# Kernel optimization log

Measured on AMD Instinct MI355X. Metric: run time of the kernel, lower is better.

Reference implementation:

```python
import jax, jax.numpy as jnp
import numpy as np

BETA = 5.0
NEG = jnp.float32(-1e30)  # finite stand-in for -inf; avoids NaN on the fully-masked row 0


def setup_inputs() -> dict:
    key = jax.random.key(0)
    ks = jax.random.split(key, 6)
    B, L, d, dv, dh = 4, 4096, 512, 512, 512
    K = jax.random.normal(ks[0], (B, L, d), dtype=jnp.float32)
    V = jax.random.normal(ks[1], (B, L, dv), dtype=jnp.float32)
    # nn.Linear weights: shape (out, in), applied as x @ W.T
    Wq = jax.random.normal(ks[2], (dh, d), dtype=jnp.float32) / np.sqrt(d).astype(np.float32)
    Wk = jax.random.normal(ks[3], (dh, d), dtype=jnp.float32) / np.sqrt(d).astype(np.float32)
    Wv = jax.random.normal(ks[4], (dv, dv), dtype=jnp.float32) / np.sqrt(dv).astype(np.float32)
    Wo = jax.random.normal(ks[5], (dv, dv), dtype=jnp.float32) / np.sqrt(dv).astype(np.float32)
    return {"K": K, "V": V, "Wq": Wq, "Wk": Wk, "Wv": Wv, "Wo": Wo}


def reference(K, V, Wq, Wk, Wv, Wo):
    B, L, _ = K.shape
    dh = Wq.shape[0]
    Qh = jnp.einsum('bld,hd->blh', K, Wq)
    Kh = jnp.einsum('bld,hd->blh', K, Wk)
    Vp = jnp.einsum('bld,ed->ble', V, Wv)
    scale = jnp.float32(BETA) / jnp.sqrt(jnp.float32(dh))
    scores = jnp.einsum('bih,bjh->bij', Qh, Kh) * scale  # [B,L,L]
    # strict causal mask: attend only to j <= i-1 (triu with diagonal=0 masked)
    mask = jnp.triu(jnp.ones((L, L), dtype=bool), k=0)
    scores = jnp.where(mask[None], NEG, scores)
    attn = jax.nn.softmax(scores, axis=-1)
    # row 0 has no past: torch code zeroes it after softmax
    attn = attn.at[:, 0, :].set(0.0)
    out = jnp.einsum('bij,bjd->bid', attn, Vp)
    Vhat = jnp.einsum('bld,ed->ble', out, Wo)
    return Vhat
```

## Files before the change

kernel.cpp:

```cpp
#include <hip/hip_runtime.h>


typedef unsigned short u16;
typedef _Float16 f16;
typedef short short8 __attribute__((ext_vector_type(8)));
typedef _Float16 half8 __attribute__((ext_vector_type(8)));
typedef _Float16 half4 __attribute__((ext_vector_type(4)));
typedef float floatx4 __attribute__((ext_vector_type(4)));

#define L_SEQ 4096
#define NBATCH 4
#define DMODEL 512
#define SCALE 0.22097086912079612f
#define MMAX 30.0f

__device__ __forceinline__ u16 f2bf(float f) {
  unsigned int u = __float_as_uint(f);
  u += 0x7fffu + ((u >> 16) & 1u);
  return (u16)(u >> 16);
}
__device__ __forceinline__ float bf2f(u16 h) {
  return __uint_as_float(((unsigned int)h) << 16);
}

__device__ __forceinline__ void gl2lds16(const void* g, void* l) {
  __builtin_amdgcn_global_load_lds(
      (const __attribute__((address_space(1))) unsigned int*)g,
      (__attribute__((address_space(3))) unsigned int*)l, 16, 0, 0);
}

__global__ __launch_bounds__(256) void cvt_f16_x4b(
    const float4* __restrict__ x0, half4* __restrict__ o0,
    const float4* __restrict__ x1, half4* __restrict__ o1, int n4a,
    const float4* __restrict__ x2, half4* __restrict__ o2,
    const float4* __restrict__ x3, half4* __restrict__ o3, int n4b) {
  int i = blockIdx.x * 256 + threadIdx.x;
  int y = blockIdx.y;
  const float4* __restrict__ x;
  half4* __restrict__ o;
  int n4;
  if (y == 0)      { x = x0; o = o0; n4 = n4a; }
  else if (y == 1) { x = x1; o = o1; n4 = n4a; }
  else if (y == 2) { x = x2; o = o2; n4 = n4b; }
  else             { x = x3; o = o3; n4 = n4b; }
  if (i >= n4) return;
  float4 f = x[i];
  half4 h = {(f16)f.x, (f16)f.y, (f16)f.z, (f16)f.w};
  o[i] = h;
}

__global__ __launch_bounds__(256) void cvt_t16(
    const float* __restrict__ x0, f16* __restrict__ o0,
    const float* __restrict__ x1, f16* __restrict__ o1) {
  const float* __restrict__ x = blockIdx.z ? x1 : x0;
  f16* __restrict__ o = blockIdx.z ? o1 : o0;
  __shared__ f16 t[64][72];
  const int r0 = blockIdx.y * 64, c0 = blockIdx.x * 64;
  const int tr = threadIdx.x >> 4, tc4 = (threadIdx.x & 15) * 4;
#pragma unroll
  for (int it = 0; it < 4; it++) {
    int r = tr + it * 16;
    float4 v = *(const float4*)&x[(long)(r0 + r) * 512 + c0 + tc4];
    t[tc4 + 0][r] = (f16)v.x;
    t[tc4 + 1][r] = (f16)v.y;
    t[tc4 + 2][r] = (f16)v.z;
    t[tc4 + 3][r] = (f16)v.w;
  }
  __syncthreads();
  const int wr = threadIdx.x >> 3, wc8 = (threadIdx.x & 7) * 8;
#pragma unroll
  for (int it = 0; it < 2; it++) {
    int rr = wr + it * 32;
    half8 h;
#pragma unroll
    for (int e = 0; e < 8; e++) h[e] = t[rr][wc8 + e];
    *(half8*)&o[(long)(c0 + rr) * 512 + r0 + wc8] = h;
  }
}

template <int OUT_MODE>
__global__ __launch_bounds__(256, 2) void gemm128(
    const f16* __restrict__ A, const f16* __restrict__ B,
    void* __restrict__ Cout, int ldc, long sAz, long sBz, long sCz) {
  __shared__ f16 sA[2][128 * 64];
  __shared__ f16 sB[2][128 * 64];

  const int tid = threadIdx.x;
  const int wave = tid >> 6, lane = tid & 63, quad = lane >> 4, l16 = lane & 15;
  const int wm = (wave >> 1) * 64, wn = (wave & 1) * 64;
  const int bn = blockIdx.x * 128, bm = blockIdx.y * 128, bz = blockIdx.z;

  const f16* Ab = A + (long)bz * sAz + (long)bm * 512;
  const f16* Bb = B + (long)bz * sBz + (long)bn * 512;

  floatx4 zero = {0.f, 0.f, 0.f, 0.f};
  floatx4 acc[4][4];
#pragma unroll
  for (int mi = 0; mi < 4; mi++)
#pragma unroll
    for (int ni = 0; ni < 4; ni++) acc[mi][ni] = zero;

  const int lrow = lane >> 3;
  auto stage = [&](int bs, int ks) {
#pragma unroll
    for (int i = 0; i < 4; i++) {
      int r0 = wave * 32 + i * 8;
      int r = r0 + lrow;
      int c = ((lane & 7) - r) & 7;
      gl2lds16(Ab + (long)r * 512 + ks * 64 + c * 8, &sA[bs][r0 * 64]);
      gl2lds16(Bb + (long)r * 512 + ks * 64 + c * 8, &sB[bs][r0 * 64]);
    }
  };

  stage(0, 0);
  for (int ks = 0; ks < 8; ks++) {
    const int cur = ks & 1;
    __syncthreads();
    if (ks + 1 < 8) stage(cur ^ 1, ks + 1);

#pragma unroll
    for (int kk = 0; kk < 2; kk++) {
      half8 af[4], bf[4];
#pragma unroll
      for (int mi = 0; mi < 4; mi++) {
        int row = wm + mi * 16 + l16;
        int slot = (kk * 4 + quad + row) & 7;
        af[mi] = *(const half8*)&sA[cur][row * 64 + slot * 8];
      }
#pragma unroll
      for (int ni = 0; ni < 4; ni++) {
        int row = wn + ni * 16 + l16;
        int slot = (kk * 4 + quad + row) & 7;
        bf[ni] = *(const half8*)&sB[cur][row * 64 + slot * 8];
      }
#pragma unroll
      for (int mi = 0; mi < 4; mi++)
#pragma unroll
        for (int ni = 0; ni < 4; ni++)
          acc[mi][ni] = __builtin_amdgcn_mfma_f32_16x16x32_f16(
              af[mi], bf[ni], acc[mi][ni], 0, 0, 0);
    }
  }

#pragma unroll
  for (int mi = 0; mi < 4; mi++) {
#pragma unroll
    for (int ni = 0; ni < 4; ni++) {
#pragma unroll
      for (int rr = 0; rr < 4; rr++) {
        int row = bm + wm + mi * 16 + quad * 4 + rr;
        int col = bn + wn + ni * 16 + l16;
        long idx = (long)bz * sCz + (long)row * ldc + col;
        float v = acc[mi][ni][rr];
        if (OUT_MODE == 1) {
          ((f16*)Cout)[idx] = (f16)v;
        } else if (OUT_MODE == 3) {
          ((u16*)Cout)[idx] = f2bf(v);
        } else {
          ((float*)Cout)[idx] = v;
        }
      }
    }
  }
}

__device__ __forceinline__ int nseg_of(int qt) {
  return (qt < 12) ? ((qt + 2) >> 1) : ((qt + 4) >> 2);
}
__device__ __forceinline__ int seg_off(int qt) {
  int o = 0;
  for (int q = 2; q < qt; q++) o += 4 * nseg_of(q);
  return o;
}

#define SV_LD 40

__global__ __launch_bounds__(512, 2) void attn_kernel(
    const f16* __restrict__ Qh_g, const f16* __restrict__ Kh_g,
    const u16* __restrict__ VpT, f16* __restrict__ Ob,
    u16* __restrict__ Opart, float* __restrict__ ml) {
  __shared__ f16 sK[2][32 * 512];
  __shared__ u16 sV[2][512 * 32];
  __shared__ u16 sP[8 * 16 * SV_LD];
  __shared__ float sL[128];

  const int tid = threadIdx.x;
  const int wave = tid >> 6, lane = tid & 63, quad = lane >> 4, l16 = lane & 15;

  int id = blockIdx.x;
  int qt = 31;
  for (;;) {
    int c = 4 * nseg_of(qt);
    if (id < c) break;
    id -= c;
    qt--;
  }
  const int S = nseg_of(qt);
  const int b = id / S;
  const int s = id - b * S;
  const int ktn = 4 * qt + 4;
  const int base = ktn / S, rem = ktn - base * S;
  const int len = base + (s < rem);
  const int start = s * base + (s < rem ? s : rem);

  const int q0 = qt * 128 + wave * 16;
  const long qbase = (long)b * L_SEQ + q0;

  half8 qf[16];
#pragma unroll
  for (int c = 0; c < 16; c++) {
    long a = (qbase + l16) * 512 + c * 32 + quad * 8;
    qf[c] = *(const half8*)&Qh_g[a];
  }

  floatx4 zero = {0.f, 0.f, 0.f, 0.f};
  float l_run[4] = {0.f, 0.f, 0.f, 0.f};
  floatx4 oacc[32];
#pragma unroll
  for (int nb = 0; nb < 32; nb++) oacc[nb] = zero;

  const f16* __restrict__ Kh_b = Kh_g + (long)b * L_SEQ * 512;
  const u16* __restrict__ V_b  = VpT + (long)b * (512L * L_SEQ);

  auto stage = [&](int bs, int jt) {
    const int j0 = jt * 32;
#pragma unroll
    for (int i = 0; i < 4; i++) {
      int r = wave * 4 + i;
      int k = (lane - (r & 7)) & 63;
      gl2lds16(Kh_b + (long)(j0 + r) * 512 + k * 8, &sK[bs][r * 512]);
    }
#pragma unroll
    for (int i = 0; i < 4; i++) {
      int g = wave * 4 + i;
      int d = g * 16 + (lane >> 2);
      int c = ((lane & 3) - (d + (d >> 2))) & 3;
      gl2lds16(V_b + (long)d * L_SEQ + j0 + c * 8, &sV[bs][g * 512]);
    }
  };

  stage(0, start);

  for (int v = 0; v < len; v++) {
    const int j0 = (start + v) * 32;
    const int cur = v & 1;

    __syncthreads();
    if (v + 1 < len) stage(cur ^ 1, start + v + 1);

    const f16* kc = &sK[cur][0];
    const u16* vc = &sV[cur][0];

    floatx4 sacc0 = zero, sacc1 = zero;
    const int rot = l16 & 7;
#pragma unroll
    for (int c = 0; c < 16; c++) {
      int slot = (c * 4 + quad + rot) & 63;
      half8 b0 = *(const half8*)&kc[l16 * 512 + slot * 8];
      half8 b1 = *(const half8*)&kc[(16 + l16) * 512 + slot * 8];
      sacc0 = __builtin_amdgcn_mfma_f32_16x16x32_f16(qf[c], b0, sacc0, 0, 0, 0);
      sacc1 = __builtin_amdgcn_mfma_f32_16x16x32_f16(qf[c], b1, sacc1, 0, 0, 0);
    }

#pragma unroll
    for (int rr = 0; rr < 4; rr++) {
      int irow = q0 + quad * 4 + rr;
      float s0 = fmaf(sacc0[rr], SCALE, -MMAX);
      float s1 = fmaf(sacc1[rr], SCALE, -MMAX);
      if (j0 + l16 >= irow) s0 = -1e30f;
      if (j0 + 16 + l16 >= irow) s1 = -1e30f;
      float p0 = __expf(s0);
      float p1 = __expf(s1);
      l_run[rr] += p0 + p1;
      int pb = wave * (16 * SV_LD) + (quad * 4 + rr) * SV_LD;
      sP[pb + l16] = f2bf(p0);
      sP[pb + 16 + l16] = f2bf(p1);
    }

    __builtin_amdgcn_sched_barrier(0);
    __builtin_amdgcn_s_waitcnt(0xC07F);
    __builtin_amdgcn_s_barrier();
    __builtin_amdgcn_sched_barrier(0);

    short8 vf[4];
#pragma unroll
    for (int nbl = 0; nbl < 4; nbl++) {
      int dvr = wave * 64 + nbl * 16 + l16;
      vf[nbl] = *(const short8*)&vc[dvr * 32 + ((quad + l16 + (l16 >> 2)) & 3) * 8];
    }
#pragma unroll
    for (int qg = 0; qg < 8; qg++) {
      short8 ap = *(const short8*)&sP[qg * (16 * SV_LD) + l16 * SV_LD + quad * 8];
#pragma unroll
      for (int nbl = 0; nbl < 4; nbl++)
        oacc[qg * 4 + nbl] =
            __builtin_amdgcn_mfma_f32_16x16x32_bf16(ap, vf[nbl], oacc[qg * 4 + nbl], 0, 0, 0);
    }
  }

#pragma unroll
  for (int rr = 0; rr < 4; rr++) {
    float l = l_run[rr];
    l += __shfl_xor(l, 1);
    l += __shfl_xor(l, 2);
    l += __shfl_xor(l, 4);
    l += __shfl_xor(l, 8);
    l_run[rr] = l;
  }
  if (l16 == 0) {
#pragma unroll
    for (int rr = 0; rr < 4; rr++) sL[wave * 16 + quad * 4 + rr] = l_run[rr];
  }
  __syncthreads();

  if (S == 1) {
#pragma unroll
    for (int qg = 0; qg < 8; qg++) {
#pragma unroll
      for (int rr = 0; rr < 4; rr++) {
        int row = qg * 16 + quad * 4 + rr;
        int irow = qt * 128 + row;
        float lv = sL[row];
        float inv = (irow == 0 || lv <= 0.f) ? 0.f : 1.0f / lv;
        long obase = ((long)b * L_SEQ + irow) * 512 + wave * 64;
#pragma unroll
        for (int nbl = 0; nbl < 4; nbl++)
          Ob[obase + nbl * 16 + l16] = (f16)(oacc[qg * 4 + nbl][rr] * inv);
      }
    }
  } else {
    const int slot = seg_off(qt) + b * S + s;
    const long obase0 = (long)slot * (128 * 512);
#pragma unroll
    for (int qg = 0; qg < 8; qg++) {
#pragma unroll
      for (int rr = 0; rr < 4; rr++) {
        int row = qg * 16 + quad * 4 + rr;
        long ob = obase0 + (long)row * 512 + wave * 64;
#pragma unroll
        for (int nbl = 0; nbl < 4; nbl++)
          Opart[ob + nbl * 16 + l16] = f2bf(oacc[qg * 4 + nbl][rr]);
      }
    }
    if (l16 == 0) {
#pragma unroll
      for (int rr = 0; rr < 4; rr++)
        ml[slot * 128 + wave * 16 + quad * 4 + rr] = l_run[rr];
    }
  }
}

__global__ __launch_bounds__(256) void attn_combine(
    const u16* __restrict__ Opart, const float* __restrict__ ml,
    f16* __restrict__ Ob) {
  const int qt = 2 + (blockIdx.x >> 2), b = blockIdx.x & 3;
  const int S = nseg_of(qt);
  const int bslot = seg_off(qt) + b * S;
  __shared__ float sInv[128];
  const int tid = threadIdx.x;
  if (tid < 128) {
    int row = tid, irow = qt * 128 + row;
    float ltot = 0.f;
    for (int s = 0; s < S; s++) ltot += ml[(bslot + s) * 128 + row];
    sInv[row] = (irow == 0 || ltot <= 0.f) ? 0.f : 1.0f / ltot;
  }
  __syncthreads();
  const int c0 = blockIdx.y * 16;
  for (int idx = tid; idx < 128 * 16; idx += 256) {
    int row = idx >> 4, cc = c0 + (idx & 15);
    float acc[8] = {0, 0, 0, 0, 0, 0, 0, 0};
    for (int s = 0; s < S; s++) {
      int4 pk = *(const int4*)&Opart[(long)(bslot + s) * 65536 + row * 512 + cc * 8];
      const u16* ph = (const u16*)&pk;
#pragma unroll
      for (int e = 0; e < 8; e++) acc[e] += bf2f(ph[e]);
    }
    float inv = sInv[row];
    f16 o[8];
#pragma unroll
    for (int e = 0; e < 8; e++) o[e] = (f16)(acc[e] * inv);
    *(int4*)&Ob[((long)b * L_SEQ + qt * 128 + row) * 512 + cc * 8] = *(int4*)o;
  }
}

extern "C" void kernel_launch(void* const* d_in, const int* in_sizes, int n_in,
                              void* d_out, int out_size, void* d_ws, size_t ws_size,
                              hipStream_t stream) {
  const float* K  = (const float*)d_in[0];
  const float* V  = (const float*)d_in[1];
  const float* Wq = (const float*)d_in[2];
  const float* Wk = (const float*)d_in[3];
  const float* Wv = (const float*)d_in[4];
  const float* Wo = (const float*)d_in[5];
  float* out = (float*)d_out;

  const int NKV = NBATCH * L_SEQ * DMODEL;
  const int NW = DMODEL * DMODEL;
  const int NSLOT = 640;

  char* w = (char*)d_ws;
  size_t off = 0;
  auto carve = [&](size_t bytes) {
    void* p = w + off;
    off += (bytes + 255) & ~(size_t)255;
    return p;
  };
  f16* Qh   = (f16*)carve((size_t)NKV * 2);
  f16* K16  = (f16*)carve((size_t)NKV * 2);
  u16* VpTw = (u16*)carve((size_t)NKV * 2);
  f16* Obw  = (f16*)carve((size_t)NKV * 2);
  f16* Wo16 = (f16*)carve((size_t)NW * 2);
  f16* MTw  = (f16*)carve((size_t)NW * 2);
  float* mlw = (float*)carve((size_t)NSLOT * 128 * 4);
  u16* Opart = (u16*)carve((size_t)NSLOT * 65536 * 2);
  f16* V16   = (f16*)Opart;
  f16* WqT16 = V16 + NKV;
  f16* WkT16 = WqT16 + NW;
  f16* Wv16  = WkT16 + NW;

  cvt_f16_x4b<<<dim3(NKV / 1024, 4, 1), 256, 0, stream>>>(
      (const float4*)K, (half4*)K16, (const float4*)V, (half4*)V16, NKV / 4,
      (const float4*)Wv, (half4*)Wv16, (const float4*)Wo, (half4*)Wo16, NW / 4);
  cvt_t16<<<dim3(8, 8, 2), 256, 0, stream>>>(Wq, WqT16, Wk, WkT16);

  gemm128<1><<<dim3(4, 4, 1), 256, 0, stream>>>(
      WkT16, WqT16, (void*)MTw, 512, 0, 0, 0);

  gemm128<1><<<dim3(4, 128, 1), 256, 0, stream>>>(
      K16, MTw, (void*)Qh, 512, 0, 0, 0);

  gemm128<3><<<dim3(32, 4, NBATCH), 256, 0, stream>>>(
      Wv16, V16, (void*)VpTw, L_SEQ, 0, (long)L_SEQ * 512, (long)512 * L_SEQ);

  attn_kernel<<<dim3(648, 1, 1), 512, 0, stream>>>(
      Qh, K16, VpTw, Obw, Opart, mlw);
  attn_combine<<<dim3(120, 4, 1), 256, 0, stream>>>(Opart, mlw, Obw);

  gemm128<2><<<dim3(4, 128, 1), 256, 0, stream>>>(
      Obw, Wo16, (void*)out, 512, 0, 0, 0);

  (void)in_sizes; (void)n_in; (void)out_size; (void)ws_size;
}
```

Measured before the change: 350.2 us.

## Fuse split-KV combine into attention via atomic counters and merge projection GEMMs

Removes the separate attn_combine launch: the last-arriving segment block for each (query tile, batch) detects completion with an atomic counter after a threadfence and performs the reduction itself. It also merges the Qh and Vp^T projection GEMMs into one grid, and moves the small weight conversions plus counter reset into one kernel. Fewer launches and better tail filling are the goal. The cost is an atomic, extra fences, and serialized reduction work on the last block per group.

```diff
diff --git a/kernel.cpp b/kernel.cpp
--- a/kernel.cpp
+++ b/kernel.cpp
@@ -29,34 +29,41 @@
       (__attribute__((address_space(3))) unsigned int*)l, 16, 0, 0);
 }
 
-__global__ __launch_bounds__(256) void cvt_f16_x4b(
+__global__ __launch_bounds__(256) void cvt_big(
     const float4* __restrict__ x0, half4* __restrict__ o0,
-    const float4* __restrict__ x1, half4* __restrict__ o1, int n4a,
-    const float4* __restrict__ x2, half4* __restrict__ o2,
-    const float4* __restrict__ x3, half4* __restrict__ o3, int n4b) {
+    const float4* __restrict__ x1, half4* __restrict__ o1, int n4) {
   int i = blockIdx.x * 256 + threadIdx.x;
-  int y = blockIdx.y;
-  const float4* __restrict__ x;
-  half4* __restrict__ o;
-  int n4;
-  if (y == 0)      { x = x0; o = o0; n4 = n4a; }
-  else if (y == 1) { x = x1; o = o1; n4 = n4a; }
-  else if (y == 2) { x = x2; o = o2; n4 = n4b; }
-  else             { x = x3; o = o3; n4 = n4b; }
   if (i >= n4) return;
+  const float4* __restrict__ x = blockIdx.y ? x1 : x0;
+  half4* __restrict__ o = blockIdx.y ? o1 : o0;
   float4 f = x[i];
   half4 h = {(f16)f.x, (f16)f.y, (f16)f.z, (f16)f.w};
   o[i] = h;
 }
 
-__global__ __launch_bounds__(256) void cvt_t16(
-    const float* __restrict__ x0, f16* __restrict__ o0,
-    const float* __restrict__ x1, f16* __restrict__ o1) {
-  const float* __restrict__ x = blockIdx.z ? x1 : x0;
-  f16* __restrict__ o = blockIdx.z ? o1 : o0;
+__global__ __launch_bounds__(256) void cvt_small(
+    const float* __restrict__ Wv, f16* __restrict__ Wv16,
+    const float* __restrict__ Wo, f16* __restrict__ Wo16,
+    const float* __restrict__ Wq, f16* __restrict__ WqT16,
+    const float* __restrict__ Wk, f16* __restrict__ WkT16,
+    int* __restrict__ cnt) {
   __shared__ f16 t[64][72];
-  const int r0 = blockIdx.y * 64, c0 = blockIdx.x * 64;
-  const int tr = threadIdx.x >> 4, tc4 = (threadIdx.x & 15) * 4;
+  const int y = blockIdx.y, bx = blockIdx.x, tid = threadIdx.x;
+  if (y == 0 && bx == 0 && tid < 128) cnt[tid] = 0;
+  if (y < 2) {
+    const float4* __restrict__ x = (const float4*)(y ? Wo : Wv);
+    half4* __restrict__ o = (half4*)(y ? Wo16 : Wv16);
+    int i = bx * 256 + tid;
+    float4 f = x[i];
+    half4 h = {(f16)f.x, (f16)f.y, (f16)f.z, (f16)f.w};
+    o[i] = h;
+    return;
+  }
+  if (bx >= 64) return;
+  const float* __restrict__ x = (y == 2) ? Wq : Wk;
+  f16* __restrict__ o = (y == 2) ? WqT16 : WkT16;
+  const int r0 = (bx >> 3) * 64, c0 = (bx & 7) * 64;
+  const int tr = tid >> 4, tc4 = (tid & 15) * 4;
 #pragma unroll
   for (int it = 0; it < 4; it++) {
     int r = tr + it * 16;
@@ -67,7 +74,7 @@
     t[tc4 + 3][r] = (f16)v.w;
   }
   __syncthreads();
-  const int wr = threadIdx.x >> 3, wc8 = (threadIdx.x & 7) * 8;
+  const int wr = tid >> 3, wc8 = (tid & 7) * 8;
 #pragma unroll
   for (int it = 0; it < 2; it++) {
     int rr = wr + it * 32;
@@ -81,17 +88,17 @@
 template <int OUT_MODE>
 __global__ __launch_bounds__(256, 2) void gemm128(
     const f16* __restrict__ A, const f16* __restrict__ B,
-    void* __restrict__ Cout, int ldc, long sAz, long sBz, long sCz) {
+    void* __restrict__ Cout, int ldc) {
   __shared__ f16 sA[2][128 * 64];
   __shared__ f16 sB[2][128 * 64];
 
   const int tid = threadIdx.x;
   const int wave = tid >> 6, lane = tid & 63, quad = lane >> 4, l16 = lane & 15;
   const int wm = (wave >> 1) * 64, wn = (wave & 1) * 64;
-  const int bn = blockIdx.x * 128, bm = blockIdx.y * 128, bz = blockIdx.z;
-
-  const f16* Ab = A + (long)bz * sAz + (long)bm * 512;
-  const f16* Bb = B + (long)bz * sBz + (long)bn * 512;
+  const int bn = blockIdx.x * 128, bm = blockIdx.y * 128;
+
+  const f16* Ab = A + (long)bm * 512;
+  const f16* Bb = B + (long)bn * 512;
 
   floatx4 zero = {0.f, 0.f, 0.f, 0.f};
   floatx4 acc[4][4];
@@ -150,15 +157,103 @@
       for (int rr = 0; rr < 4; rr++) {
         int row = bm + wm + mi * 16 + quad * 4 + rr;
         int col = bn + wn + ni * 16 + l16;
-        long idx = (long)bz * sCz + (long)row * ldc + col;
+        long idx = (long)row * ldc + col;
         float v = acc[mi][ni][rr];
-        if (OUT_MODE == 1) {
-          ((f16*)Cout)[idx] = (f16)v;
-        } else if (OUT_MODE == 3) {
-          ((u16*)Cout)[idx] = f2bf(v);
-        } else {
-          ((float*)Cout)[idx] = v;
-        }
+        if (OUT_MODE == 1) ((f16*)Cout)[idx] = (f16)v;
+        else               ((float*)Cout)[idx] = v;
+      }
+    }
+  }
+}
+
+__global__ __launch_bounds__(256, 2) void gemm_dual(
+    const f16* __restrict__ A0, const f16* __restrict__ B0, f16* __restrict__ C0,
+    const f16* __restrict__ A1, const f16* __restrict__ B1, u16* __restrict__ C1) {
+  __shared__ f16 sA[2][128 * 64];
+  __shared__ f16 sB[2][128 * 64];
+
+  const int tid = threadIdx.x;
+  const int wave = tid >> 6, lane = tid & 63, quad = lane >> 4, l16 = lane & 15;
+  const int wm = (wave >> 1) * 64, wn = (wave & 1) * 64;
+
+  const bool isT = blockIdx.x < 512;
+  int bn, bm, ldc;
+  long cbase = 0;
+  const f16 *Ab, *Bb;
+  if (isT) {
+    int id = blockIdx.x;
+    bn = (id & 3) * 128; bm = (id >> 2) * 128; ldc = 512;
+    Ab = A0 + (long)bm * 512;
+    Bb = B0 + (long)bn * 512;
+  } else {
+    int id = blockIdx.x - 512;
+    int bz = id >> 7, rem = id & 127;
+    bn = (rem & 31) * 128; bm = (rem >> 5) * 128; ldc = L_SEQ;
+    Ab = A1 + (long)bm * 512;
+    Bb = B1 + (long)bz * (L_SEQ * 512) + (long)bn * 512;
+    cbase = (long)bz * (512L * L_SEQ);
+  }
+
+  floatx4 zero = {0.f, 0.f, 0.f, 0.f};
+  floatx4 acc[4][4];
+#pragma unroll
+  for (int mi = 0; mi < 4; mi++)
+#pragma unroll
+    for (int ni = 0; ni < 4; ni++) acc[mi][ni] = zero;
+
+  const int lrow = lane >> 3;
+  auto stage = [&](int bs, int ks) {
+#pragma unroll
+    for (int i = 0; i < 4; i++) {
+      int r0 = wave * 32 + i * 8;
+      int r = r0 + lrow;
+      int c = ((lane & 7) - r) & 7;
+      gl2lds16(Ab + (long)r * 512 + ks * 64 + c * 8, &sA[bs][r0 * 64]);
+      gl2lds16(Bb + (long)r * 512 + ks * 64 + c * 8, &sB[bs][r0 * 64]);
+    }
+  };
+
+  stage(0, 0);
+  for (int ks = 0; ks < 8; ks++) {
+    const int cur = ks & 1;
+    __syncthreads();
+    if (ks + 1 < 8) stage(cur ^ 1, ks + 1);
+
+#pragma unroll
+    for (int kk = 0; kk < 2; kk++) {
+      half8 af[4], bf[4];
+#pragma unroll
+      for (int mi = 0; mi < 4; mi++) {
+        int row = wm + mi * 16 + l16;
+        int slot = (kk * 4 + quad + row) & 7;
+        af[mi] = *(const half8*)&sA[cur][row * 64 + slot * 8];
+      }
+#pragma unroll
+      for (int ni = 0; ni < 4; ni++) {
+        int row = wn + ni * 16 + l16;
+        int slot = (kk * 4 + quad + row) & 7;
+        bf[ni] = *(const half8*)&sB[cur][row * 64 + slot * 8];
+      }
+#pragma unroll
+      for (int mi = 0; mi < 4; mi++)
+#pragma unroll
+        for (int ni = 0; ni < 4; ni++)
+          acc[mi][ni] = __builtin_amdgcn_mfma_f32_16x16x32_f16(
+              af[mi], bf[ni], acc[mi][ni], 0, 0, 0);
+    }
+  }
+
+#pragma unroll
+  for (int mi = 0; mi < 4; mi++) {
+#pragma unroll
+    for (int ni = 0; ni < 4; ni++) {
+#pragma unroll
+      for (int rr = 0; rr < 4; rr++) {
+        int row = bm + wm + mi * 16 + quad * 4 + rr;
+        int col = bn + wn + ni * 16 + l16;
+        float v = acc[mi][ni][rr];
+        if (isT) C0[(long)row * ldc + col] = (f16)v;
+        else     C1[cbase + (long)row * ldc + col] = f2bf(v);
       }
     }
   }
@@ -178,11 +273,12 @@
 __global__ __launch_bounds__(512, 2) void attn_kernel(
     const f16* __restrict__ Qh_g, const f16* __restrict__ Kh_g,
     const u16* __restrict__ VpT, f16* __restrict__ Ob,
-    u16* __restrict__ Opart, float* __restrict__ ml) {
+    u16* __restrict__ Opart, float* __restrict__ ml, int* __restrict__ cnt) {
   __shared__ f16 sK[2][32 * 512];
   __shared__ u16 sV[2][512 * 32];
   __shared__ u16 sP[8 * 16 * SV_LD];
   __shared__ float sL[128];
+  __shared__ int sFlag;
 
   const int tid = threadIdx.x;
   const int wave = tid >> 6, lane = tid & 63, quad = lane >> 4, l16 = lane & 15;
@@ -328,54 +424,53 @@
           Ob[obase + nbl * 16 + l16] = (f16)(oacc[qg * 4 + nbl][rr] * inv);
       }
     }
-  } else {
-    const int slot = seg_off(qt) + b * S + s;
-    const long obase0 = (long)slot * (128 * 512);
-#pragma unroll
-    for (int qg = 0; qg < 8; qg++) {
-#pragma unroll
-      for (int rr = 0; rr < 4; rr++) {
-        int row = qg * 16 + quad * 4 + rr;
-        long ob = obase0 + (long)row * 512 + wave * 64;
-#pragma unroll
-        for (int nbl = 0; nbl < 4; nbl++)
-          Opart[ob + nbl * 16 + l16] = f2bf(oacc[qg * 4 + nbl][rr]);
-      }
-    }
-    if (l16 == 0) {
-#pragma unroll
-      for (int rr = 0; rr < 4; rr++)
-        ml[slot * 128 + wave * 16 + quad * 4 + rr] = l_run[rr];
-    }
-  }
-}
-
-__global__ __launch_bounds__(256) void attn_combine(
-    const u16* __restrict__ Opart, const float* __restrict__ ml,
-    f16* __restrict__ Ob) {
-  const int qt = 2 + (blockIdx.x >> 2), b = blockIdx.x & 3;
-  const int S = nseg_of(qt);
+    return;
+  }
+
+  const int slot = seg_off(qt) + b * S + s;
+  const long obase0 = (long)slot * (128 * 512);
+#pragma unroll
+  for (int qg = 0; qg < 8; qg++) {
+#pragma unroll
+    for (int rr = 0; rr < 4; rr++) {
+      int row = qg * 16 + quad * 4 + rr;
+      long ob = obase0 + (long)row * 512 + wave * 64;
+#pragma unroll
+      for (int nbl = 0; nbl < 4; nbl++)
+        Opart[ob + nbl * 16 + l16] = f2bf(oacc[qg * 4 + nbl][rr]);
+    }
+  }
+  if (l16 == 0) {
+#pragma unroll
+    for (int rr = 0; rr < 4; rr++)
+      ml[slot * 128 + wave * 16 + quad * 4 + rr] = l_run[rr];
+  }
+
+  __threadfence();
+  __syncthreads();
+  if (tid == 0) sFlag = atomicAdd(&cnt[(qt - 2) * 4 + b], 1);
+  __syncthreads();
+  if (sFlag != S - 1) return;
+  __threadfence();
+
   const int bslot = seg_off(qt) + b * S;
-  __shared__ float sInv[128];
-  const int tid = threadIdx.x;
   if (tid < 128) {
     int row = tid, irow = qt * 128 + row;
     float ltot = 0.f;
-    for (int s = 0; s < S; s++) ltot += ml[(bslot + s) * 128 + row];
-    sInv[row] = (irow == 0 || ltot <= 0.f) ? 0.f : 1.0f / ltot;
+    for (int si = 0; si < S; si++) ltot += ml[(bslot + si) * 128 + row];
+    sL[row] = (irow == 0 || ltot <= 0.f) ? 0.f : 1.0f / ltot;
   }
   __syncthreads();
-  const int c0 = blockIdx.y * 16;
-  for (int idx = tid; idx < 128 * 16; idx += 256) {
-    int row = idx >> 4, cc = c0 + (idx & 15);
+  for (int idx = tid; idx < 128 * 64; idx += 512) {
+    int row = idx >> 6, cc = idx & 63;
     float acc[8] = {0, 0, 0, 0, 0, 0, 0, 0};
-    for (int s = 0; s < S; s++) {
-      int4 pk = *(const int4*)&Opart[(long)(bslot + s) * 65536 + row * 512 + cc * 8];
+    for (int si = 0; si < S; si++) {
+      int4 pk = *(const int4*)&Opart[(long)(bslot + si) * 65536 + row * 512 + cc * 8];
       const u16* ph = (const u16*)&pk;
 #pragma unroll
       for (int e = 0; e < 8; e++) acc[e] += bf2f(ph[e]);
     }
-    float inv = sInv[row];
+    float inv = sL[row];
     f16 o[8];
 #pragma unroll
     for (int e = 0; e < 8; e++) o[e] = (f16)(acc[e] * inv);
@@ -412,32 +507,27 @@
   f16* Wo16 = (f16*)carve((size_t)NW * 2);
   f16* MTw  = (f16*)carve((size_t)NW * 2);
   float* mlw = (float*)carve((size_t)NSLOT * 128 * 4);
+  int* cntw  = (int*)carve(128 * 4);
   u16* Opart = (u16*)carve((size_t)NSLOT * 65536 * 2);
   f16* V16   = (f16*)Opart;
   f16* WqT16 = V16 + NKV;
   f16* WkT16 = WqT16 + NW;
   f16* Wv16  = WkT16 + NW;
 
-  cvt_f16_x4b<<<dim3(NKV / 1024, 4, 1), 256, 0, stream>>>(
-      (const float4*)K, (half4*)K16, (const float4*)V, (half4*)V16, NKV / 4,
-      (const float4*)Wv, (half4*)Wv16, (const float4*)Wo, (half4*)Wo16, NW / 4);
-  cvt_t16<<<dim3(8, 8, 2), 256, 0, stream>>>(Wq, WqT16, Wk, WkT16);
-
-  gemm128<1><<<dim3(4, 4, 1), 256, 0, stream>>>(
-      WkT16, WqT16, (void*)MTw, 512, 0, 0, 0);
-
-  gemm128<1><<<dim3(4, 128, 1), 256, 0, stream>>>(
-      K16, MTw, (void*)Qh, 512, 0, 0, 0);
-
-  gemm128<3><<<dim3(32, 4, NBATCH), 256, 0, stream>>>(
-      Wv16, V16, (void*)VpTw, L_SEQ, 0, (long)L_SEQ * 512, (long)512 * L_SEQ);
+  cvt_big<<<dim3(NKV / 1024, 2, 1), 256, 0, stream>>>(
+      (const float4*)K, (half4*)K16, (const float4*)V, (half4*)V16, NKV / 4);
+  cvt_small<<<dim3(256, 4, 1), 256, 0, stream>>>(
+      Wv, Wv16, Wo, Wo16, Wq, WqT16, Wk, WkT16, cntw);
+
+  gemm128<1><<<dim3(4, 4, 1), 256, 0, stream>>>(WkT16, WqT16, (void*)MTw, 512);
+
+  gemm_dual<<<dim3(1024, 1, 1), 256, 0, stream>>>(
+      K16, MTw, Qh, Wv16, V16, VpTw);
 
   attn_kernel<<<dim3(648, 1, 1), 512, 0, stream>>>(
-      Qh, K16, VpTw, Obw, Opart, mlw);
-  attn_combine<<<dim3(120, 4, 1), 256, 0, stream>>>(Opart, mlw, Obw);
-
-  gemm128<2><<<dim3(4, 128, 1), 256, 0, stream>>>(
-      Obw, Wo16, (void*)out, 512, 0, 0, 0);
+      Qh, K16, VpTw, Obw, Opart, mlw, cntw);
+
+  gemm128<2><<<dim3(4, 128, 1), 256, 0, stream>>>(Obw, Wo16, (void*)out, 512);
 
   (void)in_sizes; (void)n_in; (void)out_size; (void)ws_size;
 }
```

Result: slower. 650.1 us (+85.6%).
